# Kernel tuning notes

Hardware: AMD Instinct MI355X
Metric: run time of the kernel (lower is better)

## Reference

```python
import jax, jax.numpy as jnp
import numpy as np

DIM = 512
HEADS = 8
DIM_HEAD = 64  # scale constant from __init__; also dim // heads here
SCALE = DIM_HEAD ** -0.5


def setup_inputs() -> dict:
    key = jax.random.key(0)
    k1, k2, k3, k4 = jax.random.split(key, 4)
    x = jax.random.normal(k1, (2, 4096, DIM), dtype=jnp.float32)
    # nn.Linear weights: stored as [out, in]; we keep [in, out] for x @ W
    w_qkv = jax.random.normal(k2, (DIM, 3 * DIM), dtype=jnp.float32) * (DIM ** -0.5)
    w_out = jax.random.normal(k3, (DIM, DIM), dtype=jnp.float32) * (DIM ** -0.5)
    b_out = jax.random.normal(k4, (DIM,), dtype=jnp.float32) * 0.02
    return {"x": x, "w_qkv": w_qkv, "w_out": w_out, "b_out": b_out}


def reference(x, w_qkv, w_out, b_out):
    B, N, C = x.shape
    H = HEADS
    Dh = C // H
    qkv = x @ w_qkv                                   # [B, N, 3C]
    q, k, v = jnp.split(qkv, 3, axis=-1)
    # [B, N, C] -> [B, H, N, Dh]
    reshape = lambda t: t.reshape(B, N, H, Dh).transpose(0, 2, 1, 3)
    q, k, v = reshape(q), reshape(k), reshape(v)
    attn = jnp.einsum("bhnd,bhmd->bhnm", q, k) * SCALE  # [B, H, N, N]
    attn = jax.nn.softmax(attn, axis=-1)
    out = jnp.einsum("bhnm,bhmd->bhnd", attn, v)       # [B, H, N, Dh]
    out = out.transpose(0, 2, 1, 3).reshape(B, N, C)
    return out @ w_out + b_out
```

## Files before the change

### kernel.cpp

```cpp
#include <hip/hip_runtime.h>
#include <stdint.h>

typedef unsigned short u16;
typedef __bf16 bf16x8 __attribute__((ext_vector_type(8)));
typedef float fx4 __attribute__((ext_vector_type(4)));
typedef float fx16 __attribute__((ext_vector_type(16)));


__device__ __forceinline__ u16 f2bf(float f) {
    unsigned int u = __float_as_uint(f);
    u += 0x7fffu + ((u >> 16) & 1u);
    return (u16)(u >> 16);
}

__device__ __forceinline__ bf16x8 ld8(const u16* p) {
    return __builtin_bit_cast(bf16x8, *(const int4*)p);
}

__device__ __forceinline__ uint32_t pk2bf(float lo, float hi) {
    uint32_t a = __float_as_uint(lo) + 0x8000u;
    uint32_t b = __float_as_uint(hi) + 0x8000u;
    return __builtin_amdgcn_perm(b, a, 0x07060302u);
}


__global__ __launch_bounds__(256) void transpose_cast_kernel(const float* __restrict__ in,
                                                             u16* __restrict__ out,
                                                             int NR, int NC) {
    __shared__ float T[64][65];
    int t = threadIdx.x;
    int i0 = blockIdx.y * 64, j0 = blockIdx.x * 64;
    int r = t >> 4, cc = t & 15;
#pragma unroll
    for (int j = 0; j < 4; ++j) {
        int row = r + j * 16;
        float4 v = *(const float4*)(in + (size_t)(i0 + row) * NC + j0 + cc * 4);
        T[row][cc * 4 + 0] = v.x; T[row][cc * 4 + 1] = v.y;
        T[row][cc * 4 + 2] = v.z; T[row][cc * 4 + 3] = v.w;
    }
    __syncthreads();
#pragma unroll
    for (int j = 0; j < 4; ++j) {
        int jr = r + j * 16;
        unsigned int u0 = f2bf(T[cc * 4 + 0][jr]) | ((unsigned int)f2bf(T[cc * 4 + 1][jr]) << 16);
        unsigned int u1 = f2bf(T[cc * 4 + 2][jr]) | ((unsigned int)f2bf(T[cc * 4 + 3][jr]) << 16);
        uint2 u; u.x = u0; u.y = u1;
        *(uint2*)(out + (size_t)(j0 + jr) * NR + i0 + cc * 4) = u;
    }
}


#define QSCALE 0.180336880f

template<int MODE>
__global__ __launch_bounds__(256) void gemm_kernel(const void* __restrict__ Avoid,
                                                   const u16* __restrict__ Bt,
                                                   u16* __restrict__ Qf,
                                                   u16* __restrict__ Kf,
                                                   u16* __restrict__ Vf,
                                                   const float* __restrict__ bias,
                                                   float* __restrict__ Out,
                                                   int Ncols) {
    __shared__ __align__(16) u16 As[128 * 32];
    __shared__ __align__(16) u16 Bs[128 * 32];
    int tid = threadIdx.x;
    int w = tid >> 6, lane = tid & 63;
    int m16 = lane & 15, quad = lane >> 4;
    int ntn = Ncols / 128;
    int bx = blockIdx.x % ntn, by = blockIdx.x / ntn;
    int r0 = by * 128, c0 = bx * 128;
    int wr = w >> 1, wc = w & 1;

    fx4 acc[4][4] = {};

    for (int k0 = 0; k0 < 512; k0 += 32) {
        __syncthreads();
#pragma unroll
        for (int j = 0; j < 2; ++j) {
            int L = tid + j * 256;
            int row = L >> 2, c = L & 3;
            if (MODE == 0) {
                const float* af = (const float*)Avoid + (size_t)(r0 + row) * 512 + k0 + c * 8;
                float4 a = *(const float4*)af, b = *(const float4*)(af + 4);
                int4 v;
                v.x = (int)pk2bf(a.x, a.y); v.y = (int)pk2bf(a.z, a.w);
                v.z = (int)pk2bf(b.x, b.y); v.w = (int)pk2bf(b.z, b.w);
                *(int4*)&As[row * 32 + c * 8] = v;
            } else {
                const u16* ab = (const u16*)Avoid;
                *(int4*)&As[row * 32 + c * 8] = *(const int4*)(ab + (size_t)(r0 + row) * 512 + k0 + c * 8);
            }
            *(int4*)&Bs[row * 32 + c * 8] = *(const int4*)(Bt + (size_t)(c0 + row) * 512 + k0 + c * 8);
        }
        __syncthreads();
        bf16x8 af[4], bfr[4];
#pragma unroll
        for (int t = 0; t < 4; ++t) {
            af[t]  = ld8(&As[(wr * 64 + t * 16 + m16) * 32 + quad * 8]);
            bfr[t] = ld8(&Bs[(wc * 64 + t * 16 + m16) * 32 + quad * 8]);
        }
#pragma unroll
        for (int mt = 0; mt < 4; ++mt)
#pragma unroll
            for (int nt = 0; nt < 4; ++nt)
                acc[mt][nt] = __builtin_amdgcn_mfma_f32_16x16x32_bf16(af[mt], bfr[nt], acc[mt][nt], 0, 0, 0);
    }

#pragma unroll
    for (int mt = 0; mt < 4; ++mt) {
        int R0 = r0 + wr * 64 + mt * 16 + quad * 4;
#pragma unroll
        for (int nt = 0; nt < 4; ++nt) {
            int C = c0 + wc * 64 + nt * 16 + m16;
            if (MODE == 0) {
                int sec = C >> 9;
                int hd = (C >> 6) & 7, d = C & 63;
                int b = R0 >> 12, n0 = R0 & 4095;
                size_t hb = (size_t)(b * 8 + hd) * 262144;
                if (sec <= 1) {
                    u16* dst = (sec == 0) ? Qf : Kf;
                    float sc = (sec == 0) ? QSCALE : 1.0f;
                    size_t base = hb + (size_t)((n0 >> 5) * 4 + (d >> 4)) * 512
                                + ((d >> 3) & 1) * 256 + (n0 & 31) * 8 + (d & 7);
#pragma unroll
                    for (int r = 0; r < 4; ++r)
                        dst[base + r * 8] = f2bf(acc[mt][nt][r] * sc);
                } else {
                    size_t base = hb + (size_t)((n0 >> 6) * 8 + (d >> 5) * 4 + ((n0 >> 4) & 3)) * 512
                                + ((n0 >> 2) & 1) * 256 + (d & 31) * 8 + ((n0 >> 3) & 1) * 4;
                    unsigned int u0 = f2bf(acc[mt][nt][0]) | ((unsigned int)f2bf(acc[mt][nt][1]) << 16);
                    unsigned int u1 = f2bf(acc[mt][nt][2]) | ((unsigned int)f2bf(acc[mt][nt][3]) << 16);
                    uint2 u; u.x = u0; u.y = u1;
                    *(uint2*)(Vf + base) = u;
                }
            } else {
                float bv = bias[C];
#pragma unroll
                for (int r = 0; r < 4; ++r)
                    Out[(size_t)(R0 + r) * 512 + C] = acc[mt][nt][r] + bv;
            }
        }
    }
}


__device__ __forceinline__ void attn_iter(bf16x8 (&KC)[2][4], bf16x8 (&KN)[2][4],
                                          const bf16x8 (&qf)[4], const bf16x8& onesA,
                                          const fx16& Z,
                                          fx16& O0, fx16& O1, fx16& Lacc,
                                          const u16* __restrict__ Kh,
                                          const u16* __restrict__ Vh,
                                          int lane, int K0) {
    bf16x8 vf[2][4];
    {
        const u16* vb = Vh + (size_t)(K0 >> 6) * 4096 + lane * 8;
#pragma unroll
        for (int dt = 0; dt < 2; ++dt)
#pragma unroll
            for (int ch = 0; ch < 4; ++ch)
                vf[dt][ch] = ld8(vb + (dt * 4 + ch) * 512);
    }
    {
        int kn0 = (K0 + 64) & 4095;
        const u16* kb = Kh + (size_t)(kn0 >> 5) * 2048 + lane * 8;
#pragma unroll
        for (int dc = 0; dc < 4; ++dc) {
            KN[0][dc] = ld8(kb + dc * 512);
            KN[1][dc] = ld8(kb + 2048 + dc * 512);
        }
    }
    fx16 S0 = Z, S1 = Z;
#pragma unroll
    for (int dc = 0; dc < 4; ++dc) {
        S0 = __builtin_amdgcn_mfma_f32_32x32x16_bf16(KC[0][dc], qf[dc], S0, 0, 0, 0);
        S1 = __builtin_amdgcn_mfma_f32_32x32x16_bf16(KC[1][dc], qf[dc], S1, 0, 0, 0);
    }
    uint32_t pk0[8], pk1[8];
#pragma unroll
    for (int i = 0; i < 8; ++i) {
        pk0[i] = pk2bf(__builtin_amdgcn_exp2f(S0[2 * i]), __builtin_amdgcn_exp2f(S0[2 * i + 1]));
        pk1[i] = pk2bf(__builtin_amdgcn_exp2f(S1[2 * i]), __builtin_amdgcn_exp2f(S1[2 * i + 1]));
    }
#pragma unroll
    for (int c = 0; c < 4; ++c) {
        const uint32_t* pk = (c < 2) ? pk0 : pk1;
        int o = (c & 1) * 4;
        int4 bi; bi.x = (int)pk[o]; bi.y = (int)pk[o + 1]; bi.z = (int)pk[o + 2]; bi.w = (int)pk[o + 3];
        bf16x8 bfrag = __builtin_bit_cast(bf16x8, bi);
        O0 = __builtin_amdgcn_mfma_f32_32x32x16_bf16(vf[0][c], bfrag, O0, 0, 0, 0);
        O1 = __builtin_amdgcn_mfma_f32_32x32x16_bf16(vf[1][c], bfrag, O1, 0, 0, 0);
        Lacc = __builtin_amdgcn_mfma_f32_32x32x16_bf16(onesA, bfrag, Lacc, 0, 0, 0);
    }
}

__global__ __launch_bounds__(256, 2) void attn_kernel(const u16* __restrict__ Qf,
                                                      const u16* __restrict__ Kf,
                                                      const u16* __restrict__ Vf,
                                                      u16* __restrict__ Ob) {
    __shared__ __align__(16) u16 Eo[4 * 32 * 68];

    int tid = threadIdx.x;
    int w = tid >> 6, lane = tid & 63;
    int q32 = lane & 31, h = lane >> 5;
    int bh = ((blockIdx.x & 7) << 1) | ((blockIdx.x >> 3) & 1);
    int qt = blockIdx.x >> 4;
    int q0 = qt * 128;

    const u16* Qh = Qf + (size_t)bh * 262144;
    const u16* Kh = Kf + (size_t)bh * 262144;
    const u16* Vh = Vf + (size_t)bh * 262144;

    bf16x8 qf[4];
    {
        const u16* qb = Qh + (size_t)(qt * 4 + w) * 2048 + lane * 8;
#pragma unroll
        for (int dc = 0; dc < 4; ++dc)
            qf[dc] = ld8(qb + dc * 512);
    }

    int4 oi; oi.x = oi.y = oi.z = oi.w = 0x3F803F80;
    const bf16x8 onesA = __builtin_bit_cast(bf16x8, oi);
    const fx16 Z = {};
    fx16 O0 = {}, O1 = {}, Lacc = {};

    bf16x8 kA[2][4], kB[2][4];
    {
        const u16* kb = Kh + lane * 8;
#pragma unroll
        for (int dc = 0; dc < 4; ++dc) {
            kA[0][dc] = ld8(kb + dc * 512);
            kA[1][dc] = ld8(kb + 2048 + dc * 512);
        }
    }

    for (int k0 = 0; k0 < 4096; k0 += 128) {
        attn_iter(kA, kB, qf, onesA, Z, O0, O1, Lacc, Kh, Vh, lane, k0);
        attn_iter(kB, kA, qf, onesA, Z, O0, O1, Lacc, Kh, Vh, lane, k0 + 64);
    }

    float inv = 1.0f / Lacc[0];
    int ebase = w * 2176 + q32 * 68;
#pragma unroll
    for (int i = 0; i < 8; ++i) {
        int dbase = 8 * (i >> 1) + (i & 1) * 2 + 4 * h;
        uint32_t p0 = pk2bf(O0[2 * i] * inv, O0[2 * i + 1] * inv);
        uint32_t p1 = pk2bf(O1[2 * i] * inv, O1[2 * i + 1] * inv);
        *(uint32_t*)&Eo[ebase + dbase]      = p0;
        *(uint32_t*)&Eo[ebase + dbase + 32] = p1;
    }
    __syncthreads();
    int row = lane >> 1, half = lane & 1;
    int rb = w * 2176 + row * 68 + half * 32;
    int b = bh >> 3, hh = bh & 7;
    size_t gb = ((size_t)(b * 4096 + q0 + w * 32 + row)) * 512 + hh * 64 + half * 32;
#pragma unroll
    for (int s = 0; s < 4; ++s) {
        uint2 a = *(const uint2*)&Eo[rb + s * 8];
        uint2 c = *(const uint2*)&Eo[rb + s * 8 + 4];
        int4 v; v.x = (int)a.x; v.y = (int)a.y; v.z = (int)c.x; v.w = (int)c.y;
        *(int4*)(Ob + gb + s * 8) = v;
    }
}


extern "C" void kernel_launch(void* const* d_in, const int* in_sizes, int n_in,
                              void* d_out, int out_size, void* d_ws, size_t ws_size,
                              hipStream_t stream) {
    const float* x     = (const float*)d_in[0];
    const float* w_qkv = (const float*)d_in[1];
    const float* w_out = (const float*)d_in[2];
    const float* b_out = (const float*)d_in[3];
    float* out = (float*)d_out;

    char* ws = (char*)d_ws;
    u16* wqkv_t = (u16*)(ws);
    u16* wout_t = (u16*)(ws + 1572864);
    u16* Qfb    = (u16*)(ws + 2097152);
    u16* Kfb    = (u16*)(ws + 10485760);
    u16* Vfb    = (u16*)(ws + 18874368);
    u16* Ob     = (u16*)(ws + 27262976);

    transpose_cast_kernel<<<dim3(24, 8), 256, 0, stream>>>(w_qkv, wqkv_t, 512, 1536);
    transpose_cast_kernel<<<dim3(8, 8), 256, 0, stream>>>(w_out, wout_t, 512, 512);
    gemm_kernel<0><<<768, 256, 0, stream>>>(x, wqkv_t, Qfb, Kfb, Vfb, nullptr, nullptr, 1536);
    attn_kernel<<<512, 256, 0, stream>>>(Qfb, Kfb, Vfb, Ob);
    gemm_kernel<1><<<256, 256, 0, stream>>>(Ob, wout_t, nullptr, nullptr, nullptr, b_out, out, 512);
}
```

Measured before the change: 213.2 us.

## Stage GEMM epilogue through LDS, use direct global-to-LDS loads, merge transpose launches

The QKV GEMM epilogue now writes tiles into shared memory in the attention-friendly layout, then emits coalesced 16-byte global stores instead of scattered 2-byte and 8-byte stores. GEMM operand loads for bf16 inputs use global_load_lds to bypass registers. The two weight transpose launches are merged into one. An s_barrier is added to the attention loop to keep waves in lockstep for cache sharing. Together these add an extra LDS round trip and barriers in exchange for fewer uncoalesced writes and one less launch.

```diff
diff --git a/kernel.cpp b/kernel.cpp
--- a/kernel.cpp
+++ b/kernel.cpp
@@ -23,13 +23,24 @@
     return __builtin_amdgcn_perm(b, a, 0x07060302u);
 }
 
-
-__global__ __launch_bounds__(256) void transpose_cast_kernel(const float* __restrict__ in,
-                                                             u16* __restrict__ out,
-                                                             int NR, int NC) {
+typedef __attribute__((address_space(3))) uint32_t lds_u32;
+typedef __attribute__((address_space(1))) const uint32_t glb_u32;
+__device__ __forceinline__ void glds16(const u16* g, u16* l) {
+    __builtin_amdgcn_global_load_lds((glb_u32*)g, (lds_u32*)l, 16, 0, 0);
+}
+
+
+__global__ __launch_bounds__(256) void transpose_cast_kernel(const float* __restrict__ w_qkv,
+                                                             u16* __restrict__ wqkv_t,
+                                                             const float* __restrict__ w_out,
+                                                             u16* __restrict__ wout_t) {
     __shared__ float T[64][65];
     int t = threadIdx.x;
-    int i0 = blockIdx.y * 64, j0 = blockIdx.x * 64;
+    int bx = blockIdx.x;
+    const float* in; u16* out; int NR = 512, NC;
+    if (bx < 24) { in = w_qkv; out = wqkv_t; NC = 1536; }
+    else         { in = w_out; out = wout_t; NC = 512; bx -= 24; }
+    int i0 = blockIdx.y * 64, j0 = bx * 64;
     int r = t >> 4, cc = t & 15;
 #pragma unroll
     for (int j = 0; j < 4; ++j) {
@@ -61,8 +72,7 @@
                                                    const float* __restrict__ bias,
                                                    float* __restrict__ Out,
                                                    int Ncols) {
-    __shared__ __align__(16) u16 As[128 * 32];
-    __shared__ __align__(16) u16 Bs[128 * 32];
+    __shared__ __align__(16) u16 Sh[16384];
     int tid = threadIdx.x;
     int w = tid >> 6, lane = tid & 63;
     int m16 = lane & 15, quad = lane >> 4;
@@ -70,6 +80,7 @@
     int bx = blockIdx.x % ntn, by = blockIdx.x / ntn;
     int r0 = by * 128, c0 = bx * 128;
     int wr = w >> 1, wc = w & 1;
+    int lrow = lane >> 2, lchk = (lane & 3) * 8;
 
     fx4 acc[4][4] = {};
 
@@ -77,27 +88,28 @@
         __syncthreads();
 #pragma unroll
         for (int j = 0; j < 2; ++j) {
-            int L = tid + j * 256;
-            int row = L >> 2, c = L & 3;
+            int rw = j * 64 + w * 16;
             if (MODE == 0) {
+                int L = tid + j * 256;
+                int row = L >> 2, c = L & 3;
                 const float* af = (const float*)Avoid + (size_t)(r0 + row) * 512 + k0 + c * 8;
                 float4 a = *(const float4*)af, b = *(const float4*)(af + 4);
                 int4 v;
                 v.x = (int)pk2bf(a.x, a.y); v.y = (int)pk2bf(a.z, a.w);
                 v.z = (int)pk2bf(b.x, b.y); v.w = (int)pk2bf(b.z, b.w);
-                *(int4*)&As[row * 32 + c * 8] = v;
+                *(int4*)&Sh[row * 32 + c * 8] = v;
             } else {
                 const u16* ab = (const u16*)Avoid;
-                *(int4*)&As[row * 32 + c * 8] = *(const int4*)(ab + (size_t)(r0 + row) * 512 + k0 + c * 8);
+                glds16(ab + (size_t)(r0 + rw + lrow) * 512 + k0 + lchk, &Sh[rw * 32]);
             }
-            *(int4*)&Bs[row * 32 + c * 8] = *(const int4*)(Bt + (size_t)(c0 + row) * 512 + k0 + c * 8);
+            glds16(Bt + (size_t)(c0 + rw + lrow) * 512 + k0 + lchk, &Sh[4096 + rw * 32]);
         }
         __syncthreads();
         bf16x8 af[4], bfr[4];
 #pragma unroll
         for (int t = 0; t < 4; ++t) {
-            af[t]  = ld8(&As[(wr * 64 + t * 16 + m16) * 32 + quad * 8]);
-            bfr[t] = ld8(&Bs[(wc * 64 + t * 16 + m16) * 32 + quad * 8]);
+            af[t]  = ld8(&Sh[(wr * 64 + t * 16 + m16) * 32 + quad * 8]);
+            bfr[t] = ld8(&Sh[4096 + (wc * 64 + t * 16 + m16) * 32 + quad * 8]);
         }
 #pragma unroll
         for (int mt = 0; mt < 4; ++mt)
@@ -106,34 +118,52 @@
                 acc[mt][nt] = __builtin_amdgcn_mfma_f32_16x16x32_bf16(af[mt], bfr[nt], acc[mt][nt], 0, 0, 0);
     }
 
-#pragma unroll
-    for (int mt = 0; mt < 4; ++mt) {
-        int R0 = r0 + wr * 64 + mt * 16 + quad * 4;
-#pragma unroll
-        for (int nt = 0; nt < 4; ++nt) {
-            int C = c0 + wc * 64 + nt * 16 + m16;
-            if (MODE == 0) {
-                int sec = C >> 9;
-                int hd = (C >> 6) & 7, d = C & 63;
-                int b = R0 >> 12, n0 = R0 & 4095;
-                size_t hb = (size_t)(b * 8 + hd) * 262144;
-                if (sec <= 1) {
-                    u16* dst = (sec == 0) ? Qf : Kf;
-                    float sc = (sec == 0) ? QSCALE : 1.0f;
-                    size_t base = hb + (size_t)((n0 >> 5) * 4 + (d >> 4)) * 512
-                                + ((d >> 3) & 1) * 256 + (n0 & 31) * 8 + (d & 7);
+    if (MODE == 0) {
+        int sec = c0 >> 9;
+        __syncthreads();
+        if (sec <= 1) {
+            float sc = (sec == 0) ? QSCALE : 1.0f;
+#pragma unroll
+            for (int mt = 0; mt < 4; ++mt)
+#pragma unroll
+                for (int nt = 0; nt < 4; ++nt) {
+                    int lb = wc * 16 + (wr * 2 + (mt >> 1)) * 4 + nt;
+                    int eb = lb * 512 + (m16 >> 3) * 256 + ((mt & 1) * 16 + quad * 4) * 8 + (m16 & 7);
 #pragma unroll
                     for (int r = 0; r < 4; ++r)
-                        dst[base + r * 8] = f2bf(acc[mt][nt][r] * sc);
-                } else {
-                    size_t base = hb + (size_t)((n0 >> 6) * 8 + (d >> 5) * 4 + ((n0 >> 4) & 3)) * 512
-                                + ((n0 >> 2) & 1) * 256 + (d & 31) * 8 + ((n0 >> 3) & 1) * 4;
+                        Sh[eb + r * 8] = f2bf(acc[mt][nt][r] * sc);
+                }
+        } else {
+#pragma unroll
+            for (int mt = 0; mt < 4; ++mt)
+#pragma unroll
+                for (int nt = 0; nt < 4; ++nt) {
+                    int lb = wc * 16 + wr * 8 + (nt >> 1) * 4 + mt;
+                    int eb = lb * 512 + (quad & 1) * 256 + ((nt & 1) * 16 + m16) * 8 + (quad >> 1) * 4;
                     unsigned int u0 = f2bf(acc[mt][nt][0]) | ((unsigned int)f2bf(acc[mt][nt][1]) << 16);
                     unsigned int u1 = f2bf(acc[mt][nt][2]) | ((unsigned int)f2bf(acc[mt][nt][3]) << 16);
                     uint2 u; u.x = u0; u.y = u1;
-                    *(uint2*)(Vf + base) = u;
+                    *(uint2*)&Sh[eb] = u;
                 }
-            } else {
+        }
+        __syncthreads();
+        int b_ = r0 >> 12, n0 = r0 & 4095, hd0 = (c0 >> 6) & 7;
+        u16* dst; size_t gb0;
+        if (sec == 0)      { dst = Qf; gb0 = (size_t)(n0 >> 5) * 2048; }
+        else if (sec == 1) { dst = Kf; gb0 = (size_t)(n0 >> 5) * 2048; }
+        else               { dst = Vf; gb0 = (size_t)(n0 >> 6) * 4096; }
+        int hl = tid >> 7;
+        size_t gbase = (size_t)(b_ * 8 + hd0 + hl) * 262144 + gb0 + (size_t)(tid & 127) * 64;
+#pragma unroll
+        for (int s = 0; s < 8; ++s)
+            *(int4*)(dst + gbase + s * 8) = *(const int4*)&Sh[tid * 64 + s * 8];
+    } else {
+#pragma unroll
+        for (int mt = 0; mt < 4; ++mt) {
+            int R0 = r0 + wr * 64 + mt * 16 + quad * 4;
+#pragma unroll
+            for (int nt = 0; nt < 4; ++nt) {
+                int C = c0 + wc * 64 + nt * 16 + m16;
                 float bv = bias[C];
 #pragma unroll
                 for (int r = 0; r < 4; ++r)
@@ -234,6 +264,7 @@
     }
 
     for (int k0 = 0; k0 < 4096; k0 += 128) {
+        asm volatile("s_barrier" ::: "memory");
         attn_iter(kA, kB, qf, onesA, Z, O0, O1, Lacc, Kh, Vh, lane, k0);
         attn_iter(kB, kA, qf, onesA, Z, O0, O1, Lacc, Kh, Vh, lane, k0 + 64);
     }
@@ -280,8 +311,7 @@
     u16* Vfb    = (u16*)(ws + 18874368);
     u16* Ob     = (u16*)(ws + 27262976);
 
-    transpose_cast_kernel<<<dim3(24, 8), 256, 0, stream>>>(w_qkv, wqkv_t, 512, 1536);
-    transpose_cast_kernel<<<dim3(8, 8), 256, 0, stream>>>(w_out, wout_t, 512, 512);
+    transpose_cast_kernel<<<dim3(32, 8), 256, 0, stream>>>(w_qkv, wqkv_t, w_out, wout_t);
     gemm_kernel<0><<<768, 256, 0, stream>>>(x, wqkv_t, Qfb, Kfb, Vfb, nullptr, nullptr, 1536);
     attn_kernel<<<512, 256, 0, stream>>>(Qfb, Kfb, Vfb, Ob);
     gemm_kernel<1><<<256, 256, 0, stream>>>(Ob, wout_t, nullptr, nullptr, nullptr, b_out, out, 512);
```

Result: slower. 220.1 us (+3.2%).
